# Optimization experiments

Hardware: AMD Instinct MI355X
Metric: run time of the kernel (lower is better)

The kernel has to match this reference:

```python
import jax, jax.numpy as jnp
import numpy as np

EPS = 1e-12  # torch F.normalize eps

def rmsnorm(x, g, dim):
    # F.normalize(x, dim=-1) * sqrt(dim) * g  (g is a learned scalar)
    n = jnp.maximum(jnp.linalg.norm(x, axis=-1, keepdims=True), EPS)
    return x / n * (dim ** 0.5) * g

def modulate(x, scale, shift):
    # x: (B,T,D); scale/shift: (B,D)
    return x * (1.0 + scale[:, None, :]) + shift[:, None, :]

def setup_inputs() -> dict:
    key = jax.random.key(0)
    ks = jax.random.split(key, 12)
    B, T, D, H = 8, 1024, 1024, 16
    Dm = 4 * D
    s = 0.02
    inp = {
        'x': jax.random.normal(ks[0], (B, T, D), jnp.float32),
        'c': jax.random.normal(ks[1], (B, D), jnp.float32),
        'g1': jnp.ones((1,), jnp.float32),
        'g2': jnp.ones((1,), jnp.float32),
        'gq': jnp.ones((1,), jnp.float32),
        'gk': jnp.ones((1,), jnp.float32),
        'Wqkv': jax.random.normal(ks[2], (3 * D, D), jnp.float32) * s,
        'bqkv': jnp.zeros((3 * D,), jnp.float32),
        'Wproj': jax.random.normal(ks[3], (D, D), jnp.float32) * s,
        'bproj': jnp.zeros((D,), jnp.float32),
        'Wfc1': jax.random.normal(ks[4], (Dm, D), jnp.float32) * s,
        'bfc1': jnp.zeros((Dm,), jnp.float32),
        'Wfc2': jax.random.normal(ks[5], (D, Dm), jnp.float32) * s,
        'bfc2': jnp.zeros((D,), jnp.float32),
        'Wada': jax.random.normal(ks[6], (6 * D, D), jnp.float32) * s,
        'bada': jnp.zeros((6 * D,), jnp.float32),
    }
    return inp

def reference(x, c, g1, g2, gq, gk, Wqkv, bqkv, Wproj, bproj,
              Wfc1, bfc1, Wfc2, bfc2, Wada, bada):
    B, T, D = x.shape
    H = 16
    hd = D // H

    # adaLN modulation: SiLU -> Linear -> chunk 6 along last dim
    ada = jax.nn.silu(c) @ Wada.T + bada  # (B, 6D)
    shift_msa, scale_msa, gate_msa, shift_mlp, scale_mlp, gate_mlp = jnp.split(ada, 6, axis=-1)

    # --- attention branch ---
    h = modulate(rmsnorm(x, g1, D), scale_msa, shift_msa)  # (B,T,D)
    qkv = h @ Wqkv.T + bqkv  # (B,T,3D)
    qkv = qkv.reshape(B, T, 3, H, hd).transpose(2, 0, 3, 1, 4)  # (3,B,H,T,hd)
    q, k, v = qkv[0], qkv[1], qkv[2]
    q = rmsnorm(q, gq, hd) * (hd ** -0.5)
    k = rmsnorm(k, gk, hd)
    attn = jax.nn.softmax(jnp.einsum('bhqd,bhkd->bhqk', q, k), axis=-1)
    o = jnp.einsum('bhqk,bhkd->bhqd', attn, v)  # (B,H,T,hd)
    o = o.transpose(0, 2, 1, 3).reshape(B, T, D)
    o = o @ Wproj.T + bproj
    x = x + gate_msa[:, None, :] * o

    # --- MLP branch ---
    h = modulate(rmsnorm(x, g2, D), scale_mlp, shift_mlp)
    h = jax.nn.gelu(h @ Wfc1.T + bfc1, approximate=True)
    h = h @ Wfc2.T + bfc2
    x = x + gate_mlp[:, None, :] * h
    return x
```

## Files before the change

### kernel.cpp

```cpp
#include <hip/hip_runtime.h>
#include <hip/hip_bf16.h>
#include <math.h>

typedef __bf16 bf16x8 __attribute__((ext_vector_type(8)));
typedef __bf16 bf16x4 __attribute__((ext_vector_type(4)));
typedef float  f32x4  __attribute__((ext_vector_type(4)));

#define DEV static __device__ __forceinline__

DEV unsigned short f2bf(float f) {
    unsigned u = __builtin_bit_cast(unsigned, f);
    u += 0x7fffu + ((u >> 16) & 1u);
    return (unsigned short)(u >> 16);
}
DEV float bf2f(unsigned short u) {
    unsigned x = ((unsigned)u) << 16;
    return __builtin_bit_cast(float, x);
}

__global__ void k_cvt(const float* __restrict__ in, unsigned short* __restrict__ out) {
    int i = (blockIdx.x * 256 + threadIdx.x) * 4;
    float4 v = *(const float4*)(in + i);
    ushort4 o;
    o.x = f2bf(v.x); o.y = f2bf(v.y); o.z = f2bf(v.z); o.w = f2bf(v.w);
    *(ushort4*)(out + i) = o;
}

__global__ void k_ada(const float* __restrict__ c, const float* __restrict__ Wada,
                      const float* __restrict__ bada, float* __restrict__ ada) {
    __shared__ float sc[1024];
    int b = blockIdx.x;
    int tid = threadIdx.x;
    for (int k = tid; k < 1024; k += 256) {
        float x = c[b * 1024 + k];
        sc[k] = x / (1.f + __expf(-x));
    }
    __syncthreads();
    int wid = tid >> 6, lane = tid & 63;
    int n = blockIdx.y * 4 + wid;
    const float* wr = Wada + (size_t)n * 1024;
    float acc = 0.f;
    #pragma unroll
    for (int k = 0; k < 1024; k += 64) acc += sc[k + lane] * wr[k + lane];
    #pragma unroll
    for (int o = 32; o; o >>= 1) acc += __shfl_xor(acc, o);
    if (lane == 0) ada[b * 6144 + n] = acc + bada[n];
}

__global__ void k_norm_mod(const float* __restrict__ x, const float* __restrict__ ada,
                           const float* __restrict__ g, unsigned short* __restrict__ h,
                           int shift_off, int scale_off) {
    int row = blockIdx.x;
    int b = row >> 10;
    int tid = threadIdx.x;
    float4 v = *(const float4*)(x + (size_t)row * 1024 + tid * 4);
    float ss = v.x * v.x + v.y * v.y + v.z * v.z + v.w * v.w;
    #pragma unroll
    for (int o = 32; o; o >>= 1) ss += __shfl_xor(ss, o);
    __shared__ float red[4];
    int wid = tid >> 6, lane = tid & 63;
    if (lane == 0) red[wid] = ss;
    __syncthreads();
    float nrm = sqrtf(red[0] + red[1] + red[2] + red[3]);
    float f = g[0] * 32.f / fmaxf(nrm, 1e-12f);
    float4 s4 = *(const float4*)(ada + b * 6144 + scale_off + tid * 4);
    float4 h4 = *(const float4*)(ada + b * 6144 + shift_off + tid * 4);
    ushort4 o;
    o.x = f2bf(v.x * f * (1.f + s4.x) + h4.x);
    o.y = f2bf(v.y * f * (1.f + s4.y) + h4.y);
    o.z = f2bf(v.z * f * (1.f + s4.z) + h4.z);
    o.w = f2bf(v.w * f * (1.f + s4.w) + h4.w);
    *(ushort4*)(h + (size_t)row * 1024 + tid * 4) = o;
}

template <int EPI, int BN>
__global__ __launch_bounds__(512, 2)
void k_gemm2(const unsigned short* __restrict__ A, const unsigned short* __restrict__ Bw,
             const float* __restrict__ bias, int N, int K, int gridM,
             float* __restrict__ outF, unsigned short* __restrict__ outH,
             const float* __restrict__ resid, const float* __restrict__ ada, int gate_off) {
    constexpr int WN = (BN == 256) ? 4 : 2;
    constexpr int WM = 8 / WN;
    constexpr int WR = 256 / WM;
    constexpr int MF = WR / 16;
    constexpr int MF2 = MF / 2;
    constexpr int LB = BN / 128;
    constexpr int TL = 2 + LB;
    __shared__ unsigned short sA[4][256 * 32];
    __shared__ unsigned short sB[4][BN * 32];

    int tid = threadIdx.x;
    int wid = tid >> 6, lane = tid & 63;
    int li = lane & 15, lg = lane >> 4;

    int bid = blockIdx.x;
    int mb = bid % gridM, nb = bid / gridM;
    int m0 = mb * 256, n0 = nb * BN;

    int wr = (wid / WN) * WR, wc = (wid % WN) * 64;

    int arow = tid >> 2, ag = tid & 3;
    int afr = (arow & 3) ^ ((arow >> 2) & 3);
    int ags = (ag ^ afr) * 8;
    int lfr = (li & 3) ^ ((li >> 2) & 3);
    int aoff = li * 32 + ((lg ^ lfr) * 8);

    auto stageA = [&](int t) {
        int slot = t & 3;
        int kk = t << 5;
        #pragma unroll
        for (int l = 0; l < 2; ++l) {
            int row = arow + l * 128;
            const unsigned short* src = A + (size_t)(m0 + row) * K + kk + ags;
            unsigned short* dst = &sA[slot][0] + (l * 512 + wid * 64) * 8;
            __builtin_amdgcn_global_load_lds((const __attribute__((address_space(1))) void*)src,
                                             (__attribute__((address_space(3))) void*)dst, 16, 0, 0);
        }
    };
    auto stageB = [&](int t) {
        int slot = t & 3;
        int kk = t << 5;
        #pragma unroll
        for (int l = 0; l < LB; ++l) {
            int row = arow + l * 128;
            const unsigned short* src = Bw + (size_t)(n0 + row) * K + kk + ags;
            unsigned short* dst = &sB[slot][0] + (l * 512 + wid * 64) * 8;
            __builtin_amdgcn_global_load_lds((const __attribute__((address_space(1))) void*)src,
                                             (__attribute__((address_space(3))) void*)dst, 16, 0, 0);
        }
    };

    int NT = K >> 5;
    stageA(0); stageB(0); stageA(1); stageB(1); stageA(2); stageB(2);
    asm volatile("s_waitcnt vmcnt(%0)" :: "n"(2 * TL) : "memory");
    __builtin_amdgcn_s_barrier();

    f32x4 acc[MF][4] = {};

    for (int t = 0; t < NT; ++t) {
        int slot = t & 3;
        const unsigned short* pa = &sA[slot][0];
        const unsigned short* pb = &sB[slot][0];
        bf16x8 bfr[4];
        bf16x8 af[MF2];
        if (t + 3 < NT) stageA(t + 3);
        #pragma unroll
        for (int nf = 0; nf < 4; ++nf)
            bfr[nf] = *(const bf16x8*)(pb + (wc + nf * 16) * 32 + aoff);
        #pragma unroll
        for (int m = 0; m < MF2; ++m)
            af[m] = *(const bf16x8*)(pa + (wr + m * 16) * 32 + aoff);
        __builtin_amdgcn_s_barrier();
        __builtin_amdgcn_s_setprio(1);
        #pragma unroll
        for (int m = 0; m < MF2; ++m)
            #pragma unroll
            for (int nf = 0; nf < 4; ++nf)
                acc[m][nf] = __builtin_amdgcn_mfma_f32_16x16x32_bf16(af[m], bfr[nf], acc[m][nf], 0, 0, 0);
        __builtin_amdgcn_s_setprio(0);
        if (t + 3 < NT) stageB(t + 3);
        #pragma unroll
        for (int m = 0; m < MF2; ++m)
            af[m] = *(const bf16x8*)(pa + (wr + (MF2 + m) * 16) * 32 + aoff);
        __builtin_amdgcn_s_barrier();
        __builtin_amdgcn_s_setprio(1);
        #pragma unroll
        for (int m = 0; m < MF2; ++m)
            #pragma unroll
            for (int nf = 0; nf < 4; ++nf)
                acc[MF2 + m][nf] = __builtin_amdgcn_mfma_f32_16x16x32_bf16(af[m], bfr[nf], acc[MF2 + m][nf], 0, 0, 0);
        __builtin_amdgcn_s_setprio(0);
        if (t < NT - 3)       asm volatile("s_waitcnt vmcnt(%0)" :: "n"(2 * TL) : "memory");
        else if (t == NT - 3) asm volatile("s_waitcnt vmcnt(%0)" :: "n"(TL) : "memory");
        else if (t == NT - 2) asm volatile("s_waitcnt vmcnt(0)" ::: "memory");
        __builtin_amdgcn_s_barrier();
    }

    int rb4 = lg * 4;
    #pragma unroll
    for (int mf = 0; mf < MF; ++mf) {
        #pragma unroll
        for (int nf = 0; nf < 4; ++nf) {
            #pragma unroll
            for (int r = 0; r < 4; ++r) {
                int row = m0 + wr + mf * 16 + rb4 + r;
                int col = n0 + wc + nf * 16 + li;
                float vv = acc[mf][nf][r] + bias[col];
                if (EPI == 0) {
                    outH[(size_t)row * N + col] = f2bf(vv);
                } else if (EPI == 2) {
                    float a2 = 0.7978845608f * (vv + 0.044715f * vv * vv * vv);
                    float e = __expf(-2.f * fabsf(a2));
                    float th = copysignf((1.f - e) / (1.f + e), a2);
                    outH[(size_t)row * N + col] = f2bf(0.5f * vv * (1.f + th));
                } else {
                    int b = row >> 10;
                    float gt = ada[b * 6144 + gate_off + col];
                    outF[(size_t)row * N + col] = resid[(size_t)row * N + col] + gt * vv;
                }
            }
        }
    }
}

__global__ __launch_bounds__(256)
void k_qkv_post(const unsigned short* __restrict__ qkv,
                const float* __restrict__ gq, const float* __restrict__ gk,
                unsigned short* __restrict__ Qb, unsigned short* __restrict__ Kb,
                unsigned short* __restrict__ Vtg) {
    __shared__ unsigned short vt[64 * 72];
    int bh = blockIdx.x;
    int b = bh >> 4, h = bh & 15;
    int t0 = blockIdx.y * 64;
    int tid = threadIdx.x;
    int row = tid >> 2, part = tid & 3;
    size_t rbase = ((size_t)(b * 1024 + t0 + row)) * 3072 + h * 64 + part * 16;
    size_t obase = (size_t)bh * 65536 + (size_t)(t0 + row) * 64 + part * 16;

    #pragma unroll
    for (int s = 0; s < 2; ++s) {
        uint4 u0 = *(const uint4*)(qkv + rbase + s * 1024);
        uint4 u1 = *(const uint4*)(qkv + rbase + s * 1024 + 8);
        float vals[16];
        const unsigned* pu = (const unsigned*)&u0;
        #pragma unroll
        for (int j = 0; j < 4; ++j) {
            vals[2*j]   = bf2f((unsigned short)(pu[j] & 0xffff));
            vals[2*j+1] = bf2f((unsigned short)(pu[j] >> 16));
        }
        pu = (const unsigned*)&u1;
        #pragma unroll
        for (int j = 0; j < 4; ++j) {
            vals[8+2*j]   = bf2f((unsigned short)(pu[j] & 0xffff));
            vals[8+2*j+1] = bf2f((unsigned short)(pu[j] >> 16));
        }
        float ss = 0.f;
        #pragma unroll
        for (int j = 0; j < 16; ++j) ss += vals[j] * vals[j];
        ss += __shfl_xor(ss, 1);
        ss += __shfl_xor(ss, 2);
        float nrm = fmaxf(sqrtf(ss), 1e-12f);
        float fsc = (s == 0 ? gq[0] : 8.f * gk[0]) / nrm;
        uint4 w0, w1;
        unsigned* pw = (unsigned*)&w0;
        #pragma unroll
        for (int j = 0; j < 4; ++j)
            pw[j] = (unsigned)f2bf(vals[2*j] * fsc) | ((unsigned)f2bf(vals[2*j+1] * fsc) << 16);
        pw = (unsigned*)&w1;
        #pragma unroll
        for (int j = 0; j < 4; ++j)
            pw[j] = (unsigned)f2bf(vals[8+2*j] * fsc) | ((unsigned)f2bf(vals[8+2*j+1] * fsc) << 16);
        unsigned short* dst = (s == 0 ? Qb : Kb);
        *(uint4*)(dst + obase)     = w0;
        *(uint4*)(dst + obase + 8) = w1;
    }
    {
        uint4 u0 = *(const uint4*)(qkv + rbase + 2048);
        uint4 u1 = *(const uint4*)(qkv + rbase + 2048 + 8);
        const unsigned* pu = (const unsigned*)&u0;
        #pragma unroll
        for (int j = 0; j < 4; ++j) {
            vt[(part * 16 + 2*j)     * 72 + row] = (unsigned short)(pu[j] & 0xffff);
            vt[(part * 16 + 2*j + 1) * 72 + row] = (unsigned short)(pu[j] >> 16);
        }
        pu = (const unsigned*)&u1;
        #pragma unroll
        for (int j = 0; j < 4; ++j) {
            vt[(part * 16 + 8 + 2*j)     * 72 + row] = (unsigned short)(pu[j] & 0xffff);
            vt[(part * 16 + 8 + 2*j + 1) * 72 + row] = (unsigned short)(pu[j] >> 16);
        }
    }
    __syncthreads();
    {
        int d = tid >> 2, seg = tid & 3;
        uint4 w0 = *(const uint4*)(vt + d * 72 + seg * 16);
        uint4 w1 = *(const uint4*)(vt + d * 72 + seg * 16 + 8);
        size_t vdst = (size_t)bh * 65536 + (size_t)d * 1024 + t0 + seg * 16;
        *(uint4*)(Vtg + vdst)     = w0;
        *(uint4*)(Vtg + vdst + 8) = w1;
    }
}

__global__ __launch_bounds__(256)
void k_attn_mfma(const unsigned short* __restrict__ Qb,
                 const unsigned short* __restrict__ Kb,
                 const unsigned short* __restrict__ Vtg,
                 unsigned short* __restrict__ outp) {
    __shared__ unsigned short Kt[128 * 64];
    __shared__ unsigned short Vl[64 * 136];
    int bh = blockIdx.x;
    int t0 = blockIdx.y * 64;
    int tid = threadIdx.x, wid = tid >> 6, lane = tid & 63;
    int li = lane & 15, lg = lane >> 4;
    const size_t bh64k = (size_t)bh * 65536;

    bf16x8 q0, q1;
    {
        const unsigned short* Qg = Qb + bh64k + (size_t)(t0 + wid * 16 + li) * 64 + lg * 8;
        q0 = *(const bf16x8*)Qg;
        q1 = *(const bf16x8*)(Qg + 32);
    }
    f32x4 oacc[4] = {};
    float den = 0.f;

    for (int kt = 0; kt < 8; ++kt) {
        __syncthreads();
        #pragma unroll
        for (int i = 0; i < 4; ++i) {
            int s = i * 256 + tid;
            int r = s >> 3, c16 = s & 7;
            const unsigned short* src = Kb + bh64k + (size_t)(kt * 128 + r) * 64 + ((c16 ^ (r & 7)) * 8);
            unsigned short* dst = Kt + i * 2048 + wid * 512;
            __builtin_amdgcn_global_load_lds((const __attribute__((address_space(1))) void*)src,
                                             (__attribute__((address_space(3))) void*)dst, 16, 0, 0);
        }
        #pragma unroll
        for (int i = 0; i < 4; ++i) {
            int s = i * 256 + tid;
            int d = s >> 4, k16 = s & 15;
            uint4 v = *(const uint4*)(Vtg + bh64k + (size_t)d * 1024 + kt * 128 + k16 * 8);
            *(uint4*)(Vl + d * 136 + k16 * 8) = v;
        }
        __syncthreads();

        f32x4 st[8];
        #pragma unroll
        for (int f = 0; f < 8; ++f) {
            int row = f * 16 + li;
            bf16x8 a0 = *(const bf16x8*)(Kt + row * 64 + ((lg       ^ (row & 7)) * 8));
            bf16x8 a1 = *(const bf16x8*)(Kt + row * 64 + (((4 + lg) ^ (row & 7)) * 8));
            f32x4 s = {};
            s = __builtin_amdgcn_mfma_f32_16x16x32_bf16(a0, q0, s, 0, 0, 0);
            s = __builtin_amdgcn_mfma_f32_16x16x32_bf16(a1, q1, s, 0, 0, 0);
            f32x4 e;
            e[0] = __expf(s[0]); e[1] = __expf(s[1]);
            e[2] = __expf(s[2]); e[3] = __expf(s[3]);
            den += e[0] + e[1] + e[2] + e[3];
            st[f] = e;
        }
        #pragma unroll
        for (int ks = 0; ks < 4; ++ks) {
            f32x4 e0 = st[2 * ks], e1 = st[2 * ks + 1];
            bf16x8 pa;
            pa[0] = (__bf16)e0[0]; pa[1] = (__bf16)e0[1]; pa[2] = (__bf16)e0[2]; pa[3] = (__bf16)e0[3];
            pa[4] = (__bf16)e1[0]; pa[5] = (__bf16)e1[1]; pa[6] = (__bf16)e1[2]; pa[7] = (__bf16)e1[3];
            #pragma unroll
            for (int df = 0; df < 4; ++df) {
                const unsigned short* vp = Vl + (df * 16 + li) * 136 + ks * 32 + lg * 4;
                bf16x4 v0 = *(const bf16x4*)vp;
                bf16x4 v1 = *(const bf16x4*)(vp + 16);
                bf16x8 vb = __builtin_shufflevector(v0, v1, 0, 1, 2, 3, 4, 5, 6, 7);
                oacc[df] = __builtin_amdgcn_mfma_f32_16x16x32_bf16(pa, vb, oacc[df], 0, 0, 0);
            }
        }
    }
    den += __shfl_xor(den, 16);
    den += __shfl_xor(den, 32);

    int b = bh >> 4, h = bh & 15;
    #pragma unroll
    for (int r2 = 0; r2 < 4; ++r2) {
        float dm = __shfl(den, lg * 4 + r2);
        float inv = 1.f / dm;
        int t = t0 + wid * 16 + lg * 4 + r2;
        #pragma unroll
        for (int df = 0; df < 4; ++df) {
            int col = h * 64 + df * 16 + li;
            outp[((size_t)(b * 1024 + t)) * 1024 + col] = f2bf(oacc[df][r2] * inv);
        }
    }
}

extern "C" void kernel_launch(void* const* d_in, const int* in_sizes, int n_in,
                              void* d_out, int out_size, void* d_ws, size_t ws_size,
                              hipStream_t stream) {
    const float* x     = (const float*)d_in[0];
    const float* c     = (const float*)d_in[1];
    const float* g1    = (const float*)d_in[2];
    const float* g2    = (const float*)d_in[3];
    const float* gq    = (const float*)d_in[4];
    const float* gk    = (const float*)d_in[5];
    const float* Wqkv  = (const float*)d_in[6];
    const float* bqkv  = (const float*)d_in[7];
    const float* Wproj = (const float*)d_in[8];
    const float* bproj = (const float*)d_in[9];
    const float* Wfc1  = (const float*)d_in[10];
    const float* bfc1  = (const float*)d_in[11];
    const float* Wfc2  = (const float*)d_in[12];
    const float* bfc2  = (const float*)d_in[13];
    const float* Wada  = (const float*)d_in[14];
    const float* bada  = (const float*)d_in[15];
    float* out = (float*)d_out;

    char* ws = (char*)d_ws;
    unsigned short* wqkv_bf = (unsigned short*)ws; ws += (size_t)3072 * 1024 * 2;
    unsigned short* wproj_bf= (unsigned short*)ws; ws += (size_t)1024 * 1024 * 2;
    unsigned short* wfc1_bf = (unsigned short*)ws; ws += (size_t)4096 * 1024 * 2;
    unsigned short* wfc2_bf = (unsigned short*)ws; ws += (size_t)4096 * 1024 * 2;
    float* ada = (float*)ws;                       ws += (size_t)8 * 6144 * 4;
    unsigned short* hbuf = (unsigned short*)ws;    ws += (size_t)8192 * 1024 * 2;
    unsigned short* qkvb16 = (unsigned short*)ws;  ws += (size_t)8192 * 3072 * 2;
    unsigned short* Qb  = (unsigned short*)ws;     ws += (size_t)8192 * 64 * 16 * 2;
    unsigned short* Kb  = (unsigned short*)ws;     ws += (size_t)8192 * 64 * 16 * 2;
    unsigned short* Vtg = (unsigned short*)ws;     ws += (size_t)8192 * 64 * 16 * 2;
    unsigned short* fc1out = qkvb16;

    k_cvt<<<3072 * 1024 / 1024, 256, 0, stream>>>(Wqkv,  wqkv_bf);
    k_cvt<<<1024 * 1024 / 1024, 256, 0, stream>>>(Wproj, wproj_bf);
    k_cvt<<<4096 * 1024 / 1024, 256, 0, stream>>>(Wfc1,  wfc1_bf);
    k_cvt<<<4096 * 1024 / 1024, 256, 0, stream>>>(Wfc2,  wfc2_bf);
    k_ada<<<dim3(8, 1536), 256, 0, stream>>>(c, Wada, bada, ada);
    k_norm_mod<<<8192, 256, 0, stream>>>(x, ada, g1, hbuf, 0, 1024);
    k_gemm2<0, 256><<<384, 512, 0, stream>>>(hbuf, wqkv_bf, bqkv, 3072, 1024, 32,
                                             nullptr, qkvb16, nullptr, nullptr, 0);
    k_qkv_post<<<dim3(128, 16), 256, 0, stream>>>(qkvb16, gq, gk, Qb, Kb, Vtg);
    k_attn_mfma<<<dim3(128, 16), 256, 0, stream>>>(Qb, Kb, Vtg, hbuf);
    k_gemm2<1, 128><<<256, 512, 0, stream>>>(hbuf, wproj_bf, bproj, 1024, 1024, 32,
                                             out, nullptr, x, ada, 2048);
    k_norm_mod<<<8192, 256, 0, stream>>>(out, ada, g2, hbuf, 3072, 4096);
    k_gemm2<2, 256><<<512, 512, 0, stream>>>(hbuf, wfc1_bf, bfc1, 4096, 1024, 32,
                                             nullptr, fc1out, nullptr, nullptr, 0);
    k_gemm2<3, 128><<<256, 512, 0, stream>>>(fc1out, wfc2_bf, bfc2, 1024, 4096, 32,
                                             out, nullptr, out, ada, 5120);
}
```

Baseline: 477.7 us.

## Rewrite GEMM with BK=64, triple buffering and uniform 256x128 tiles

Replaces the templated GEMM with one kernel that uses a 256x128 block tile for all four projections. It doubles the K step to 64, goes from a 4-deep to a 3-deep shared-memory ring, and changes the XOR swizzle to match the wider rows. Warps are now laid out 2x4 with 128x32 sub-tiles. The aim is fewer barriers and loop iterations per K and more blocks for the QKV and FC1 GEMMs. In exchange, the QKV and FC1 tiles are smaller, which lowers operand reuse and means more global traffic per FLOP, and the shallower prefetch may expose more latency.

```diff
diff --git a/kernel.cpp b/kernel.cpp
--- a/kernel.cpp
+++ b/kernel.cpp
@@ -73,117 +73,119 @@
     *(ushort4*)(h + (size_t)row * 1024 + tid * 4) = o;
 }
 
-template <int EPI, int BN>
+template <int EPI>
 __global__ __launch_bounds__(512, 2)
-void k_gemm2(const unsigned short* __restrict__ A, const unsigned short* __restrict__ Bw,
-             const float* __restrict__ bias, int N, int K, int gridM,
+void k_gemm3(const unsigned short* __restrict__ A, const unsigned short* __restrict__ Bw,
+             const float* __restrict__ bias, int N, int K,
              float* __restrict__ outF, unsigned short* __restrict__ outH,
              const float* __restrict__ resid, const float* __restrict__ ada, int gate_off) {
-    constexpr int WN = (BN == 256) ? 4 : 2;
-    constexpr int WM = 8 / WN;
-    constexpr int WR = 256 / WM;
-    constexpr int MF = WR / 16;
-    constexpr int MF2 = MF / 2;
-    constexpr int LB = BN / 128;
-    constexpr int TL = 2 + LB;
-    __shared__ unsigned short sA[4][256 * 32];
-    __shared__ unsigned short sB[4][BN * 32];
+    constexpr int ASZ = 2 * 128 * 64;
+    constexpr int BSZ = 128 * 64;
+    __shared__ unsigned short sA[3][ASZ];
+    __shared__ unsigned short sB[3][BSZ];
 
     int tid = threadIdx.x;
     int wid = tid >> 6, lane = tid & 63;
     int li = lane & 15, lg = lane >> 4;
-
     int bid = blockIdx.x;
-    int mb = bid % gridM, nb = bid / gridM;
-    int m0 = mb * 256, n0 = nb * BN;
-
-    int wr = (wid / WN) * WR, wc = (wid % WN) * 64;
-
-    int arow = tid >> 2, ag = tid & 3;
-    int afr = (arow & 3) ^ ((arow >> 2) & 3);
-    int ags = (ag ^ afr) * 8;
-    int lfr = (li & 3) ^ ((li >> 2) & 3);
-    int aoff = li * 32 + ((lg ^ lfr) * 8);
+    int mb = bid & 31, nb = bid >> 5;
+    int m0 = mb * 256, n0 = nb * 128;
+    int wc = (wid & 3) * 32;
+
+    int trow = tid >> 3;
+    int gcol = ((tid & 7) ^ (trow & 7)) * 8;
+    int sx = li & 7;
+    int abase = (wid >> 2) * 8192 + li * 64;
+    int g0 = (lg ^ sx) * 8;
+    int g1 = ((4 + lg) ^ sx) * 8;
 
     auto stageA = [&](int t) {
-        int slot = t & 3;
-        int kk = t << 5;
-        #pragma unroll
-        for (int l = 0; l < 2; ++l) {
-            int row = arow + l * 128;
-            const unsigned short* src = A + (size_t)(m0 + row) * K + kk + ags;
-            unsigned short* dst = &sA[slot][0] + (l * 512 + wid * 64) * 8;
+        int buf = t % 3; int kk = t << 6;
+        #pragma unroll
+        for (int l = 0; l < 4; ++l) {
+            const unsigned short* src = A + (size_t)(m0 + l * 64 + trow) * K + kk + gcol;
+            unsigned short* dst = &sA[buf][0] + (l * 512 + wid * 64) * 8;
             __builtin_amdgcn_global_load_lds((const __attribute__((address_space(1))) void*)src,
                                              (__attribute__((address_space(3))) void*)dst, 16, 0, 0);
         }
     };
     auto stageB = [&](int t) {
-        int slot = t & 3;
-        int kk = t << 5;
-        #pragma unroll
-        for (int l = 0; l < LB; ++l) {
-            int row = arow + l * 128;
-            const unsigned short* src = Bw + (size_t)(n0 + row) * K + kk + ags;
-            unsigned short* dst = &sB[slot][0] + (l * 512 + wid * 64) * 8;
+        int buf = t % 3; int kk = t << 6;
+        #pragma unroll
+        for (int l = 0; l < 2; ++l) {
+            const unsigned short* src = Bw + (size_t)(n0 + l * 64 + trow) * K + kk + gcol;
+            unsigned short* dst = &sB[buf][0] + (l * 512 + wid * 64) * 8;
             __builtin_amdgcn_global_load_lds((const __attribute__((address_space(1))) void*)src,
                                              (__attribute__((address_space(3))) void*)dst, 16, 0, 0);
         }
     };
 
-    int NT = K >> 5;
-    stageA(0); stageB(0); stageA(1); stageB(1); stageA(2); stageB(2);
-    asm volatile("s_waitcnt vmcnt(%0)" :: "n"(2 * TL) : "memory");
+    int NT = K >> 6;
+    stageA(0); stageB(0); stageA(1); stageB(1);
+    asm volatile("s_waitcnt vmcnt(6)" ::: "memory");
     __builtin_amdgcn_s_barrier();
 
-    f32x4 acc[MF][4] = {};
+    f32x4 acc[8][2] = {};
 
     for (int t = 0; t < NT; ++t) {
-        int slot = t & 3;
-        const unsigned short* pa = &sA[slot][0];
-        const unsigned short* pb = &sB[slot][0];
-        bf16x8 bfr[4];
-        bf16x8 af[MF2];
-        if (t + 3 < NT) stageA(t + 3);
-        #pragma unroll
-        for (int nf = 0; nf < 4; ++nf)
-            bfr[nf] = *(const bf16x8*)(pb + (wc + nf * 16) * 32 + aoff);
-        #pragma unroll
-        for (int m = 0; m < MF2; ++m)
-            af[m] = *(const bf16x8*)(pa + (wr + m * 16) * 32 + aoff);
+        int buf = t % 3;
+        const unsigned short* pa = &sA[buf][0];
+        const unsigned short* pb = &sB[buf][0];
+        bool pre = (t + 2 < NT);
+        bf16x8 bfr[2][2];
+        #pragma unroll
+        for (int nf = 0; nf < 2; ++nf) {
+            int rb = (wc + nf * 16 + li) * 64;
+            bfr[nf][0] = *(const bf16x8*)(pb + rb + g0);
+            bfr[nf][1] = *(const bf16x8*)(pb + rb + g1);
+        }
+        bf16x8 afr[4][2];
+        #pragma unroll
+        for (int mf = 0; mf < 4; ++mf) {
+            afr[mf][0] = *(const bf16x8*)(pa + abase + mf * 1024 + g0);
+            afr[mf][1] = *(const bf16x8*)(pa + abase + mf * 1024 + g1);
+        }
+        if (pre) stageA(t + 2);
         __builtin_amdgcn_s_barrier();
         __builtin_amdgcn_s_setprio(1);
         #pragma unroll
-        for (int m = 0; m < MF2; ++m)
+        for (int mf = 0; mf < 4; ++mf)
             #pragma unroll
-            for (int nf = 0; nf < 4; ++nf)
-                acc[m][nf] = __builtin_amdgcn_mfma_f32_16x16x32_bf16(af[m], bfr[nf], acc[m][nf], 0, 0, 0);
+            for (int nf = 0; nf < 2; ++nf) {
+                acc[mf][nf] = __builtin_amdgcn_mfma_f32_16x16x32_bf16(afr[mf][0], bfr[nf][0], acc[mf][nf], 0, 0, 0);
+                acc[mf][nf] = __builtin_amdgcn_mfma_f32_16x16x32_bf16(afr[mf][1], bfr[nf][1], acc[mf][nf], 0, 0, 0);
+            }
         __builtin_amdgcn_s_setprio(0);
-        if (t + 3 < NT) stageB(t + 3);
-        #pragma unroll
-        for (int m = 0; m < MF2; ++m)
-            af[m] = *(const bf16x8*)(pa + (wr + (MF2 + m) * 16) * 32 + aoff);
+        #pragma unroll
+        for (int mf = 0; mf < 4; ++mf) {
+            afr[mf][0] = *(const bf16x8*)(pa + abase + (4 + mf) * 1024 + g0);
+            afr[mf][1] = *(const bf16x8*)(pa + abase + (4 + mf) * 1024 + g1);
+        }
+        if (pre) stageB(t + 2);
         __builtin_amdgcn_s_barrier();
         __builtin_amdgcn_s_setprio(1);
         #pragma unroll
-        for (int m = 0; m < MF2; ++m)
+        for (int mf = 0; mf < 4; ++mf)
             #pragma unroll
-            for (int nf = 0; nf < 4; ++nf)
-                acc[MF2 + m][nf] = __builtin_amdgcn_mfma_f32_16x16x32_bf16(af[m], bfr[nf], acc[MF2 + m][nf], 0, 0, 0);
+            for (int nf = 0; nf < 2; ++nf) {
+                acc[4 + mf][nf] = __builtin_amdgcn_mfma_f32_16x16x32_bf16(afr[mf][0], bfr[nf][0], acc[4 + mf][nf], 0, 0, 0);
+                acc[4 + mf][nf] = __builtin_amdgcn_mfma_f32_16x16x32_bf16(afr[mf][1], bfr[nf][1], acc[4 + mf][nf], 0, 0, 0);
+            }
         __builtin_amdgcn_s_setprio(0);
-        if (t < NT - 3)       asm volatile("s_waitcnt vmcnt(%0)" :: "n"(2 * TL) : "memory");
-        else if (t == NT - 3) asm volatile("s_waitcnt vmcnt(%0)" :: "n"(TL) : "memory");
+        if (t < NT - 2)       asm volatile("s_waitcnt vmcnt(6)" ::: "memory");
         else if (t == NT - 2) asm volatile("s_waitcnt vmcnt(0)" ::: "memory");
         __builtin_amdgcn_s_barrier();
     }
 
+    int wm = (wid >> 2) * 128;
     int rb4 = lg * 4;
     #pragma unroll
-    for (int mf = 0; mf < MF; ++mf) {
-        #pragma unroll
-        for (int nf = 0; nf < 4; ++nf) {
+    for (int mf = 0; mf < 8; ++mf) {
+        #pragma unroll
+        for (int nf = 0; nf < 2; ++nf) {
             #pragma unroll
             for (int r = 0; r < 4; ++r) {
-                int row = m0 + wr + mf * 16 + rb4 + r;
+                int row = m0 + wm + mf * 16 + rb4 + r;
                 int col = n0 + wc + nf * 16 + li;
                 float vv = acc[mf][nf][r] + bias[col];
                 if (EPI == 0) {
@@ -411,15 +413,15 @@
     k_cvt<<<4096 * 1024 / 1024, 256, 0, stream>>>(Wfc2,  wfc2_bf);
     k_ada<<<dim3(8, 1536), 256, 0, stream>>>(c, Wada, bada, ada);
     k_norm_mod<<<8192, 256, 0, stream>>>(x, ada, g1, hbuf, 0, 1024);
-    k_gemm2<0, 256><<<384, 512, 0, stream>>>(hbuf, wqkv_bf, bqkv, 3072, 1024, 32,
-                                             nullptr, qkvb16, nullptr, nullptr, 0);
+    k_gemm3<0><<<768, 512, 0, stream>>>(hbuf, wqkv_bf, bqkv, 3072, 1024,
+                                        nullptr, qkvb16, nullptr, nullptr, 0);
     k_qkv_post<<<dim3(128, 16), 256, 0, stream>>>(qkvb16, gq, gk, Qb, Kb, Vtg);
     k_attn_mfma<<<dim3(128, 16), 256, 0, stream>>>(Qb, Kb, Vtg, hbuf);
-    k_gemm2<1, 128><<<256, 512, 0, stream>>>(hbuf, wproj_bf, bproj, 1024, 1024, 32,
-                                             out, nullptr, x, ada, 2048);
+    k_gemm3<1><<<256, 512, 0, stream>>>(hbuf, wproj_bf, bproj, 1024, 1024,
+                                        out, nullptr, x, ada, 2048);
     k_norm_mod<<<8192, 256, 0, stream>>>(out, ada, g2, hbuf, 3072, 4096);
-    k_gemm2<2, 256><<<512, 512, 0, stream>>>(hbuf, wfc1_bf, bfc1, 4096, 1024, 32,
-                                             nullptr, fc1out, nullptr, nullptr, 0);
-    k_gemm2<3, 128><<<256, 512, 0, stream>>>(fc1out, wfc2_bf, bfc2, 1024, 4096, 32,
-                                             out, nullptr, out, ada, 5120);
-}
+    k_gemm3<2><<<1024, 512, 0, stream>>>(hbuf, wfc1_bf, bfc1, 4096, 1024,
+                                         nullptr, fc1out, nullptr, nullptr, 0);
+    k_gemm3<3><<<256, 512, 0, stream>>>(fc1out, wfc2_bf, bfc2, 1024, 4096,
+                                        out, nullptr, out, ada, 5120);
+}
```

Measured after the change: 430.4 us. 9.9% less time.
